# Kernel optimization log

Hardware: AMD Instinct MI355X
Metric: run time of the kernel (lower is better)

The kernel has to match this reference:

```python
import jax, jax.numpy as jnp
import numpy as np

B, L, C = 2, 4096, 1024
H, WIN = 16, 128            # num_heads, window_size (each side)
D = C // H                  # head_dim = 64


def setup_inputs() -> dict:
    key = jax.random.key(0)
    ks = jax.random.split(key, 9)
    s = 0.02
    return {
        "x": jax.random.normal(ks[0], (B, L, C), jnp.float32),
        # Linear weights stored as [in, out] (y = x @ W + b), same math as torch Linear.
        "wq": jax.random.normal(ks[1], (C, C), jnp.float32) * s,
        "bq": jnp.zeros((C,), jnp.float32),
        "wk": jax.random.normal(ks[2], (C, C), jnp.float32) * s,
        "bk": jnp.zeros((C,), jnp.float32),
        "wv": jax.random.normal(ks[3], (C, C), jnp.float32) * s,
        "bv": jnp.zeros((C,), jnp.float32),
        "wo": jax.random.normal(ks[4], (C, C), jnp.float32) * s,
        "bo": jnp.zeros((C,), jnp.float32),
    }


def reference(x, wq, bq, wk, bk, wv, bv, wo, bo):
    b, l, c = x.shape
    nb = l // WIN

    def heads(t):  # (B,L,C) -> (B,H,L,D)
        return t.reshape(b, l, H, D).transpose(0, 2, 1, 3)

    q = heads(x @ wq + bq)
    k = heads(x @ wk + bk)
    v = heads(x @ wv + bv)

    # and ARE included in the softmax, exactly as the original module does).
    kp = jnp.pad(k, ((0, 0), (0, 0), (WIN, WIN), (0, 0)))
    vp = jnp.pad(v, ((0, 0), (0, 0), (WIN, WIN), (0, 0)))

    idx = np.arange(nb)[:, None] * WIN + np.arange(3 * WIN)[None, :]  # [nb, 3W]
    kb = kp[:, :, idx]  # [B,H,nb,3W,D]
    vb = vp[:, :, idx]  # [B,H,nb,3W,D]
    qb = q.reshape(b, H, nb, WIN, D)

    scores = jnp.einsum('bhnqd,bhnkd->bhnqk', qb, kb) / float(np.sqrt(D))
    r = np.arange(WIN)[:, None]
    col = np.arange(3 * WIN)[None, :]
    band = jnp.asarray(np.abs(col - r - WIN) <= WIN)
    scores = jnp.where(band, scores, -jnp.inf)
    probs = jax.nn.softmax(scores, axis=-1)

    out = jnp.einsum('bhnqk,bhnkd->bhnqd', probs, vb)
    out = out.reshape(b, H, l, D).transpose(0, 2, 1, 3).reshape(b, l, c)
    return out @ wo + bo
```

## Files before the change

### kernel.cpp

```cpp
#include <hip/hip_runtime.h>

using short8  = __attribute__((ext_vector_type(8))) short;
using short4v = __attribute__((ext_vector_type(4))) short;
using floatx4 = __attribute__((ext_vector_type(4))) float;

#define MFMA_B16(a, b, c) __builtin_amdgcn_mfma_f32_16x16x32_bf16(a, b, c, 0, 0, 0)

__device__ __forceinline__ short f2bf(float f) {
  union { float f; unsigned u; } v; v.f = f;
  unsigned r = v.u + 0x7fffu + ((v.u >> 16) & 1u);
  return (short)(r >> 16);
}

__device__ __forceinline__ void gload_lds16(const short* g, short* l) {
  __builtin_amdgcn_global_load_lds(
      (const __attribute__((address_space(1))) unsigned int*)g,
      (__attribute__((address_space(3))) unsigned int*)l, 16, 0, 0);
}

__global__ __launch_bounds__(256) void cast_x(const float4* __restrict__ x,
                                              short4v* __restrict__ xb, int n4) {
  int i = blockIdx.x * 256 + threadIdx.x;
  if (i < n4) {
    float4 v = x[i];
    short4v o = { f2bf(v.x), f2bf(v.y), f2bf(v.z), f2bf(v.w) };
    xb[i] = o;
  }
}

__global__ __launch_bounds__(256) void transpose_cast_w(
    const float* __restrict__ w0, const float* __restrict__ w1,
    const float* __restrict__ w2, const float* __restrict__ w3,
    short* __restrict__ wT) {
  __shared__ float tile[32][33];
  int z = blockIdx.z;
  const float* w = z == 0 ? w0 : (z == 1 ? w1 : (z == 2 ? w2 : w3));
  short* out = wT + (size_t)z * 1024 * 1024;
  int n0 = blockIdx.x * 32, k0 = blockIdx.y * 32;
  int tx = threadIdx.x, ty = threadIdx.y;
#pragma unroll
  for (int i = 0; i < 4; ++i)
    tile[ty + i * 8][tx] = w[(size_t)(k0 + ty + i * 8) * 1024 + n0 + tx];
  __syncthreads();
#pragma unroll
  for (int i = 0; i < 4; ++i)
    out[(size_t)(n0 + ty + i * 8) * 1024 + k0 + tx] = f2bf(tile[tx][ty + i * 8]);
}

__global__ __launch_bounds__(256) void gemm_qkv(
    const short* __restrict__ xb, const short* __restrict__ wT,
    const float* __restrict__ bq, const float* __restrict__ bk,
    const float* __restrict__ bv, short* __restrict__ qkv) {
  const int K = 1024;
  int z = blockIdx.z;
  const short* wt = wT + (size_t)z * 1024 * 1024;
  const float* bias = z == 0 ? bq : (z == 1 ? bk : bv);
  short* out = qkv + (size_t)z * 8192 * 1024;

  int m0 = blockIdx.x * 128, n0 = blockIdx.y * 128;
  __shared__ __align__(16) short a[128][32];
  __shared__ __align__(16) short bt[128][32];
  int tid = threadIdx.x;
  int w = tid >> 6, lane = tid & 63, quad = lane >> 4, l16 = lane & 15;
  int wm = (w >> 1) * 64, wn = (w & 1) * 64;
  floatx4 zf = {0.f, 0.f, 0.f, 0.f};
  floatx4 acc[4][4];
#pragma unroll
  for (int i = 0; i < 4; ++i)
#pragma unroll
    for (int j = 0; j < 4; ++j) acc[i][j] = zf;

  int rowL = lane >> 2;
  int segL = (lane & 3) * 8;
  const short* ga = xb + (size_t)(m0 + w * 32 + rowL) * K + segL;
  const short* gb = wt + (size_t)(n0 + w * 32 + rowL) * K + segL;
  short* la = &a[w * 32][0];
  short* lb = &bt[w * 32][0];

  for (int k0 = 0; k0 < K; k0 += 32) {
    __syncthreads();
    gload_lds16(ga + k0, la);
    gload_lds16(ga + (size_t)16 * K + k0, la + 16 * 32);
    gload_lds16(gb + k0, lb);
    gload_lds16(gb + (size_t)16 * K + k0, lb + 16 * 32);
    __syncthreads();
    short8 af[4], bf[4];
#pragma unroll
    for (int t = 0; t < 4; ++t) {
      af[t] = *(const short8*)(&a[wm + t * 16 + l16][quad * 8]);
      bf[t] = *(const short8*)(&bt[wn + t * 16 + l16][quad * 8]);
    }
#pragma unroll
    for (int i = 0; i < 4; ++i)
#pragma unroll
      for (int j = 0; j < 4; ++j)
        acc[i][j] = MFMA_B16(af[i], bf[j], acc[i][j]);
  }

  if (z == 2) {
#pragma unroll
    for (int i = 0; i < 4; ++i)
#pragma unroll
      for (int j = 0; j < 4; ++j) {
        int m = m0 + wm + i * 16 + quad * 4;
        int cc = n0 + wn + j * 16 + l16;
        float bs = bias[cc];
        int b = m >> 12, l = m & 4095;
        int hh = cc >> 6, d = cc & 63;
        short4v pack;
#pragma unroll
        for (int rg = 0; rg < 4; ++rg) pack[rg] = f2bf(acc[i][j][rg] + bs);
        *(short4v*)(out + ((size_t)(b * 16 + hh) * 64 + d) * 4096 + l) = pack;
      }
  } else {
    float qs = (z == 0) ? 0.125f : 1.0f;
#pragma unroll
    for (int i = 0; i < 4; ++i)
#pragma unroll
      for (int j = 0; j < 4; ++j)
#pragma unroll
        for (int rg = 0; rg < 4; ++rg) {
          int m = m0 + wm + i * 16 + quad * 4 + rg;
          int cc = n0 + wn + j * 16 + l16;
          float v = (acc[i][j][rg] + bias[cc]) * qs;
          int b = m >> 12, l = m & 4095;
          int hh = cc >> 6, d = cc & 63;
          out[((size_t)(b * 16 + hh) * 4096 + l) * 64 + d] = f2bf(v);
        }
  }
}

__global__ __launch_bounds__(256) void attn_kern(const short* __restrict__ qkv,
                                                 short* __restrict__ attnb) {
  const int L = 4096, H = 16;
  int n = blockIdx.x, h = blockIdx.y, b = blockIdx.z;
  const size_t hs = (size_t)L * 64;
  const short* Qp = qkv + (size_t)(b * H + h) * hs;
  const short* Kp = qkv + (size_t)8192 * 1024 + (size_t)(b * H + h) * hs;
  const short* Vt = qkv + (size_t)2 * 8192 * 1024 + (size_t)(b * H + h) * hs;

  __shared__ __align__(16) short kt[128][72];
  __shared__ __align__(16) short vt[80][136];
  __shared__ __align__(16) short pl[4][32][136];

  int tid = threadIdx.x, w = tid >> 6, lane = tid & 63, quad = lane >> 4, l16 = lane & 15;

  for (int i = tid; i < 16 * 136; i += 256) {
    int rr = i / 136;
    vt[64 + rr][i - rr * 136] = (rr == 0) ? (short)0x3F80 : (short)0;
  }

  short8 qf[2][2];
#pragma unroll
  for (int rt = 0; rt < 2; ++rt)
#pragma unroll
    for (int ks = 0; ks < 2; ++ks)
      qf[rt][ks] = *(const short8*)(Qp + (size_t)(n * 128 + w * 32 + rt * 16 + l16) * 64 + ks * 32 + quad * 8);

  floatx4 zf = {0.f, 0.f, 0.f, 0.f};
  floatx4 o[2][4];
  floatx4 osum[2];
#pragma unroll
  for (int i = 0; i < 2; ++i) {
    osum[i] = zf;
#pragma unroll
    for (int j = 0; j < 4; ++j) o[i][j] = zf;
  }

#pragma unroll
  for (int c = 0; c < 3; ++c) {
    int bk = n - 1 + c;
    bool inr = (c == 1) || (c == 0 ? (n > 0) : (n < 31));
    __syncthreads();
    if (inr) {
      const short* kc_ = Kp + (size_t)bk * 128 * 64;
      int kr = tid >> 2, ksg = (tid & 3) * 16;
#pragma unroll
      for (int p = 0; p < 2; ++p) {
        int r2 = p * 64 + kr;
        *(short8*)(&kt[r2][ksg])     = *(const short8*)(kc_ + r2 * 64 + ksg);
        *(short8*)(&kt[r2][ksg + 8]) = *(const short8*)(kc_ + r2 * 64 + ksg + 8);
      }
      const short* vc_ = Vt + (size_t)bk * 128;
      int vr = tid >> 2, vsg = (tid & 3) * 32;
#pragma unroll
      for (int q2 = 0; q2 < 4; ++q2)
        *(short8*)(&vt[vr][vsg + q2 * 8]) = *(const short8*)(vc_ + (size_t)vr * 4096 + vsg + q2 * 8);
    } else {
      short8 z8 = {0, 0, 0, 0, 0, 0, 0, 0};
      int kr = tid >> 2, ksg = (tid & 3) * 16;
#pragma unroll
      for (int p = 0; p < 2; ++p) {
        int r2 = p * 64 + kr;
        *(short8*)(&kt[r2][ksg])     = z8;
        *(short8*)(&kt[r2][ksg + 8]) = z8;
      }
      int vr = tid >> 2, vsg = (tid & 3) * 32;
#pragma unroll
      for (int q2 = 0; q2 < 4; ++q2) *(short8*)(&vt[vr][vsg + q2 * 8]) = z8;
    }
    __syncthreads();

    floatx4 s[2][8];
#pragma unroll
    for (int rt = 0; rt < 2; ++rt)
#pragma unroll
      for (int ct = 0; ct < 8; ++ct) s[rt][ct] = zf;
#pragma unroll
    for (int ct = 0; ct < 8; ++ct) {
      short8 kf0 = *(const short8*)(&kt[ct * 16 + l16][quad * 8]);
      short8 kf1 = *(const short8*)(&kt[ct * 16 + l16][32 + quad * 8]);
#pragma unroll
      for (int rt = 0; rt < 2; ++rt) {
        s[rt][ct] = MFMA_B16(qf[rt][0], kf0, s[rt][ct]);
        s[rt][ct] = MFMA_B16(qf[rt][1], kf1, s[rt][ct]);
      }
    }

#pragma unroll
    for (int rt = 0; rt < 2; ++rt) {
#pragma unroll
      for (int rg = 0; rg < 4; ++rg) {
        int r = w * 32 + rt * 16 + quad * 4 + rg;
#pragma unroll
        for (int ct = 0; ct < 8; ++ct) {
          int j = ct * 16 + l16;
          float p = __expf(s[rt][ct][rg]);
          if (c == 0) p = (j < r) ? 0.f : p;
          if (c == 2) p = (j > r) ? 0.f : p;
          pl[w][rt * 16 + quad * 4 + rg][ct * 16 + l16] = f2bf(p);
        }
      }
    }

#pragma unroll
    for (int ks = 0; ks < 4; ++ks) {
      short8 vf[5];
#pragma unroll
      for (int ct = 0; ct < 4; ++ct)
        vf[ct] = *(const short8*)(&vt[ct * 16 + l16][ks * 32 + quad * 8]);
      vf[4] = *(const short8*)(&vt[64 + l16][ks * 32 + quad * 8]);
#pragma unroll
      for (int rt = 0; rt < 2; ++rt) {
        short8 pf = *(const short8*)(&pl[w][rt * 16 + l16][ks * 32 + quad * 8]);
#pragma unroll
        for (int ct = 0; ct < 4; ++ct) o[rt][ct] = MFMA_B16(pf, vf[ct], o[rt][ct]);
        osum[rt] = MFMA_B16(pf, vf[4], osum[rt]);
      }
    }
  }

#pragma unroll
  for (int rt = 0; rt < 2; ++rt) {
#pragma unroll
    for (int rg = 0; rg < 4; ++rg) {
      float ssum = __shfl(osum[rt][rg], lane & 48);
      float inv = 1.f / ssum;
      int r = n * 128 + w * 32 + rt * 16 + quad * 4 + rg;
#pragma unroll
      for (int ct = 0; ct < 4; ++ct)
        attnb[(size_t)(b * L + r) * 1024 + h * 64 + ct * 16 + l16] =
            f2bf(o[rt][ct][rg] * inv);
    }
  }
}

__global__ __launch_bounds__(256) void gemm_out(
    const short* __restrict__ attnb, const short* __restrict__ wTo,
    const float* __restrict__ bo, float* __restrict__ outp) {
  const int K = 1024;
  int m0 = blockIdx.x * 128, n0 = blockIdx.y * 128;
  __shared__ __align__(16) short a[128][32];
  __shared__ __align__(16) short bt[128][32];
  int tid = threadIdx.x;
  int w = tid >> 6, lane = tid & 63, quad = lane >> 4, l16 = lane & 15;
  int wm = (w >> 1) * 64, wn = (w & 1) * 64;
  floatx4 zf = {0.f, 0.f, 0.f, 0.f};
  floatx4 acc[4][4];
#pragma unroll
  for (int i = 0; i < 4; ++i)
#pragma unroll
    for (int j = 0; j < 4; ++j) acc[i][j] = zf;

  int rowL = lane >> 2;
  int segL = (lane & 3) * 8;
  const short* ga = attnb + (size_t)(m0 + w * 32 + rowL) * K + segL;
  const short* gb = wTo + (size_t)(n0 + w * 32 + rowL) * K + segL;
  short* la = &a[w * 32][0];
  short* lb = &bt[w * 32][0];

  for (int k0 = 0; k0 < K; k0 += 32) {
    __syncthreads();
    gload_lds16(ga + k0, la);
    gload_lds16(ga + (size_t)16 * K + k0, la + 16 * 32);
    gload_lds16(gb + k0, lb);
    gload_lds16(gb + (size_t)16 * K + k0, lb + 16 * 32);
    __syncthreads();
    short8 af[4], bf[4];
#pragma unroll
    for (int t = 0; t < 4; ++t) {
      af[t] = *(const short8*)(&a[wm + t * 16 + l16][quad * 8]);
      bf[t] = *(const short8*)(&bt[wn + t * 16 + l16][quad * 8]);
    }
#pragma unroll
    for (int i = 0; i < 4; ++i)
#pragma unroll
      for (int j = 0; j < 4; ++j)
        acc[i][j] = MFMA_B16(af[i], bf[j], acc[i][j]);
  }
#pragma unroll
  for (int i = 0; i < 4; ++i)
#pragma unroll
    for (int j = 0; j < 4; ++j)
#pragma unroll
      for (int rg = 0; rg < 4; ++rg) {
        int m = m0 + wm + i * 16 + quad * 4 + rg;
        int c = n0 + wn + j * 16 + l16;
        outp[(size_t)m * 1024 + c] = acc[i][j][rg] + bo[c];
      }
}

extern "C" void kernel_launch(void* const* d_in, const int* in_sizes, int n_in,
                              void* d_out, int out_size, void* d_ws, size_t ws_size,
                              hipStream_t stream) {
  const float* x  = (const float*)d_in[0];
  const float* wq = (const float*)d_in[1];
  const float* bq = (const float*)d_in[2];
  const float* wk = (const float*)d_in[3];
  const float* bk = (const float*)d_in[4];
  const float* wv = (const float*)d_in[5];
  const float* bv = (const float*)d_in[6];
  const float* wo = (const float*)d_in[7];
  const float* bo = (const float*)d_in[8];

  char* ws = (char*)d_ws;
  short* xb    = (short*)ws;
  short* wT    = (short*)(ws + (16u << 20));
  short* qkv   = (short*)(ws + (24u << 20));
  short* attnb = (short*)(ws + (72u << 20));

  cast_x<<<8192, 256, 0, stream>>>((const float4*)x, (short4v*)xb, 2097152);
  transpose_cast_w<<<dim3(32, 32, 4), dim3(32, 8), 0, stream>>>(wq, wk, wv, wo, wT);
  gemm_qkv<<<dim3(64, 8, 3), 256, 0, stream>>>(xb, wT, bq, bk, bv, qkv);
  attn_kern<<<dim3(32, 16, 2), 256, 0, stream>>>(qkv, attnb);
  gemm_out<<<dim3(64, 8), 256, 0, stream>>>(attnb, wT + 3u * 1024 * 1024, bo, (float*)d_out);
}
```

Baseline: 236.4 us.

## Merge prep kernels, transpose V separately, skip masked attention tiles

Fuses the x cast and the weight transpose-cast into one launch. V is now written row-major by the QKV GEMM and then transposed by a separate LDS-tiled kernel, replacing the scattered short4 stores. The attention kernel skips QK and PV MFMAs and exp work for tiles that are fully masked in the edge chunks, and writes a register-resident ones fragment for the row-sum instead of keeping it in LDS. It adds an extra launch and an extra V round trip through memory, plus a __syncthreads in the attention loop.

```diff
diff --git a/kernel.cpp b/kernel.cpp
--- a/kernel.cpp
+++ b/kernel.cpp
@@ -18,44 +18,45 @@
       (__attribute__((address_space(3))) unsigned int*)l, 16, 0, 0);
 }
 
-__global__ __launch_bounds__(256) void cast_x(const float4* __restrict__ x,
-                                              short4v* __restrict__ xb, int n4) {
-  int i = blockIdx.x * 256 + threadIdx.x;
-  if (i < n4) {
-    float4 v = x[i];
-    short4v o = { f2bf(v.x), f2bf(v.y), f2bf(v.z), f2bf(v.w) };
-    xb[i] = o;
-  }
-}
-
-__global__ __launch_bounds__(256) void transpose_cast_w(
+__global__ __launch_bounds__(256) void prep(
+    const float4* __restrict__ x, short4v* __restrict__ xb,
     const float* __restrict__ w0, const float* __restrict__ w1,
     const float* __restrict__ w2, const float* __restrict__ w3,
     short* __restrict__ wT) {
   __shared__ float tile[32][33];
-  int z = blockIdx.z;
-  const float* w = z == 0 ? w0 : (z == 1 ? w1 : (z == 2 ? w2 : w3));
-  short* out = wT + (size_t)z * 1024 * 1024;
-  int n0 = blockIdx.x * 32, k0 = blockIdx.y * 32;
-  int tx = threadIdx.x, ty = threadIdx.y;
-#pragma unroll
-  for (int i = 0; i < 4; ++i)
-    tile[ty + i * 8][tx] = w[(size_t)(k0 + ty + i * 8) * 1024 + n0 + tx];
-  __syncthreads();
-#pragma unroll
-  for (int i = 0; i < 4; ++i)
-    out[(size_t)(n0 + ty + i * 8) * 1024 + k0 + tx] = f2bf(tile[tx][ty + i * 8]);
+  int blk = blockIdx.x;
+  if (blk < 8192) {
+    int i = blk * 256 + threadIdx.x;
+    float4 v = x[i];
+    short4v o = { f2bf(v.x), f2bf(v.y), f2bf(v.z), f2bf(v.w) };
+    xb[i] = o;
+  } else {
+    int r = blk - 8192;
+    int z = r >> 10; r &= 1023;
+    const float* w = z == 0 ? w0 : (z == 1 ? w1 : (z == 2 ? w2 : w3));
+    short* out = wT + (size_t)z * 1024 * 1024;
+    int n0 = (r & 31) * 32, k0 = (r >> 5) * 32;
+    int tx = threadIdx.x & 31, ty = threadIdx.x >> 5;
+#pragma unroll
+    for (int i = 0; i < 4; ++i)
+      tile[ty + i * 8][tx] = w[(size_t)(k0 + ty + i * 8) * 1024 + n0 + tx];
+    __syncthreads();
+#pragma unroll
+    for (int i = 0; i < 4; ++i)
+      out[(size_t)(n0 + ty + i * 8) * 1024 + k0 + tx] = f2bf(tile[tx][ty + i * 8]);
+  }
 }
 
 __global__ __launch_bounds__(256) void gemm_qkv(
     const short* __restrict__ xb, const short* __restrict__ wT,
     const float* __restrict__ bq, const float* __restrict__ bk,
-    const float* __restrict__ bv, short* __restrict__ qkv) {
+    const float* __restrict__ bv, short* __restrict__ qkv,
+    short* __restrict__ vstage) {
   const int K = 1024;
   int z = blockIdx.z;
   const short* wt = wT + (size_t)z * 1024 * 1024;
   const float* bias = z == 0 ? bq : (z == 1 ? bk : bv);
-  short* out = qkv + (size_t)z * 8192 * 1024;
+  short* out = (z == 2) ? vstage : qkv + (size_t)z * 8192 * 1024;
 
   int m0 = blockIdx.x * 128, n0 = blockIdx.y * 128;
   __shared__ __align__(16) short a[128][32];
@@ -97,37 +98,39 @@
         acc[i][j] = MFMA_B16(af[i], bf[j], acc[i][j]);
   }
 
-  if (z == 2) {
-#pragma unroll
-    for (int i = 0; i < 4; ++i)
-#pragma unroll
-      for (int j = 0; j < 4; ++j) {
-        int m = m0 + wm + i * 16 + quad * 4;
+  float qs = (z == 0) ? 0.125f : 1.0f;
+#pragma unroll
+  for (int i = 0; i < 4; ++i)
+#pragma unroll
+    for (int j = 0; j < 4; ++j)
+#pragma unroll
+      for (int rg = 0; rg < 4; ++rg) {
+        int m = m0 + wm + i * 16 + quad * 4 + rg;
         int cc = n0 + wn + j * 16 + l16;
-        float bs = bias[cc];
+        float v = (acc[i][j][rg] + bias[cc]) * qs;
         int b = m >> 12, l = m & 4095;
         int hh = cc >> 6, d = cc & 63;
-        short4v pack;
-#pragma unroll
-        for (int rg = 0; rg < 4; ++rg) pack[rg] = f2bf(acc[i][j][rg] + bs);
-        *(short4v*)(out + ((size_t)(b * 16 + hh) * 64 + d) * 4096 + l) = pack;
-      }
-  } else {
-    float qs = (z == 0) ? 0.125f : 1.0f;
-#pragma unroll
-    for (int i = 0; i < 4; ++i)
-#pragma unroll
-      for (int j = 0; j < 4; ++j)
-#pragma unroll
-        for (int rg = 0; rg < 4; ++rg) {
-          int m = m0 + wm + i * 16 + quad * 4 + rg;
-          int cc = n0 + wn + j * 16 + l16;
-          float v = (acc[i][j][rg] + bias[cc]) * qs;
-          int b = m >> 12, l = m & 4095;
-          int hh = cc >> 6, d = cc & 63;
-          out[((size_t)(b * 16 + hh) * 4096 + l) * 64 + d] = f2bf(v);
-        }
-  }
+        out[((size_t)(b * 16 + hh) * 4096 + l) * 64 + d] = f2bf(v);
+      }
+}
+
+__global__ __launch_bounds__(256) void transpose_v(const short* __restrict__ vin,
+                                                   short* __restrict__ vout) {
+  __shared__ __align__(16) short t[64][72];
+  int bh = blockIdx.x >> 6;
+  int l0 = (blockIdx.x & 63) * 64;
+  const short* src = vin + ((size_t)bh * 4096 + l0) * 64;
+  int tid = threadIdx.x;
+  int row = tid >> 2, seg = (tid & 3) * 16;
+  *(short8*)(&t[row][seg])     = *(const short8*)(src + row * 64 + seg);
+  *(short8*)(&t[row][seg + 8]) = *(const short8*)(src + row * 64 + seg + 8);
+  __syncthreads();
+  short* dst = vout + (size_t)bh * 64 * 4096 + l0;
+  short8 p0, p1;
+#pragma unroll
+  for (int j = 0; j < 8; ++j) { p0[j] = t[seg + j][row]; p1[j] = t[seg + 8 + j][row]; }
+  *(short8*)(dst + (size_t)row * 4096 + seg)     = p0;
+  *(short8*)(dst + (size_t)row * 4096 + seg + 8) = p1;
 }
 
 __global__ __launch_bounds__(256) void attn_kern(const short* __restrict__ qkv,
@@ -140,14 +143,16 @@
   const short* Vt = qkv + (size_t)2 * 8192 * 1024 + (size_t)(b * H + h) * hs;
 
   __shared__ __align__(16) short kt[128][72];
-  __shared__ __align__(16) short vt[80][136];
+  __shared__ __align__(16) short vt[64][136];
   __shared__ __align__(16) short pl[4][32][136];
 
   int tid = threadIdx.x, w = tid >> 6, lane = tid & 63, quad = lane >> 4, l16 = lane & 15;
 
-  for (int i = tid; i < 16 * 136; i += 256) {
-    int rr = i / 136;
-    vt[64 + rr][i - rr * 136] = (rr == 0) ? (short)0x3F80 : (short)0;
+  short8 onesf;
+  {
+    short ov = (l16 == 0) ? (short)0x3F80 : (short)0;
+#pragma unroll
+    for (int j = 0; j < 8; ++j) onesf[j] = ov;
   }
 
   short8 qf[2][2];
@@ -208,44 +213,67 @@
       for (int ct = 0; ct < 8; ++ct) s[rt][ct] = zf;
 #pragma unroll
     for (int ct = 0; ct < 8; ++ct) {
-      short8 kf0 = *(const short8*)(&kt[ct * 16 + l16][quad * 8]);
-      short8 kf1 = *(const short8*)(&kt[ct * 16 + l16][32 + quad * 8]);
-#pragma unroll
-      for (int rt = 0; rt < 2; ++rt) {
-        s[rt][ct] = MFMA_B16(qf[rt][0], kf0, s[rt][ct]);
-        s[rt][ct] = MFMA_B16(qf[rt][1], kf1, s[rt][ct]);
+      bool any = (c == 0) ? (ct >= w * 2) : (c == 2) ? (ct <= w * 2 + 1) : true;
+      if (any) {
+        short8 kf0 = *(const short8*)(&kt[ct * 16 + l16][quad * 8]);
+        short8 kf1 = *(const short8*)(&kt[ct * 16 + l16][32 + quad * 8]);
+#pragma unroll
+        for (int rt = 0; rt < 2; ++rt) {
+          bool valid = (c == 0) ? (ct >= w * 2 + rt) : (c == 2) ? (ct <= w * 2 + rt) : true;
+          if (valid) {
+            s[rt][ct] = MFMA_B16(qf[rt][0], kf0, s[rt][ct]);
+            s[rt][ct] = MFMA_B16(qf[rt][1], kf1, s[rt][ct]);
+          }
+        }
       }
     }
 
 #pragma unroll
     for (int rt = 0; rt < 2; ++rt) {
-#pragma unroll
-      for (int rg = 0; rg < 4; ++rg) {
-        int r = w * 32 + rt * 16 + quad * 4 + rg;
-#pragma unroll
-        for (int ct = 0; ct < 8; ++ct) {
-          int j = ct * 16 + l16;
-          float p = __expf(s[rt][ct][rg]);
-          if (c == 0) p = (j < r) ? 0.f : p;
-          if (c == 2) p = (j > r) ? 0.f : p;
-          pl[w][rt * 16 + quad * 4 + rg][ct * 16 + l16] = f2bf(p);
+      int wrt = w * 2 + rt;
+#pragma unroll
+      for (int ct = 0; ct < 8; ++ct) {
+        bool tileMasked = (c == 0) ? (ct < wrt) : (c == 2) ? (ct > wrt) : false;
+        bool ksDead = (c == 0) ? (2 * (ct >> 1) + 1 < wrt)
+                    : (c == 2) ? (2 * (ct >> 1) > wrt) : false;
+        if (ksDead) continue;
+        if (tileMasked) {
+#pragma unroll
+          for (int rg = 0; rg < 4; ++rg)
+            pl[w][rt * 16 + quad * 4 + rg][ct * 16 + l16] = 0;
+        } else {
+#pragma unroll
+          for (int rg = 0; rg < 4; ++rg) {
+            int r = w * 32 + rt * 16 + quad * 4 + rg;
+            int j = ct * 16 + l16;
+            float p = __expf(s[rt][ct][rg]);
+            if (c == 0) p = (j < r) ? 0.f : p;
+            if (c == 2) p = (j > r) ? 0.f : p;
+            pl[w][rt * 16 + quad * 4 + rg][ct * 16 + l16] = f2bf(p);
+          }
         }
       }
     }
 
+    __syncthreads();
+
 #pragma unroll
     for (int ks = 0; ks < 4; ++ks) {
-      short8 vf[5];
+      bool anyrt = (c == 0) ? (2 * ks + 1 >= w * 2) : (c == 2) ? (2 * ks <= w * 2 + 1) : true;
+      if (!anyrt) continue;
+      short8 vf[4];
 #pragma unroll
       for (int ct = 0; ct < 4; ++ct)
         vf[ct] = *(const short8*)(&vt[ct * 16 + l16][ks * 32 + quad * 8]);
-      vf[4] = *(const short8*)(&vt[64 + l16][ks * 32 + quad * 8]);
 #pragma unroll
       for (int rt = 0; rt < 2; ++rt) {
+        int wrt = w * 2 + rt;
+        bool ksDead = (c == 0) ? (2 * ks + 1 < wrt) : (c == 2) ? (2 * ks > wrt) : false;
+        if (ksDead) continue;
         short8 pf = *(const short8*)(&pl[w][rt * 16 + l16][ks * 32 + quad * 8]);
 #pragma unroll
         for (int ct = 0; ct < 4; ++ct) o[rt][ct] = MFMA_B16(pf, vf[ct], o[rt][ct]);
-        osum[rt] = MFMA_B16(pf, vf[4], osum[rt]);
+        osum[rt] = MFMA_B16(pf, onesf, osum[rt]);
       }
     }
   }
@@ -334,14 +362,15 @@
   const float* bo = (const float*)d_in[8];
 
   char* ws = (char*)d_ws;
-  short* xb    = (short*)ws;
-  short* wT    = (short*)(ws + (16u << 20));
-  short* qkv   = (short*)(ws + (24u << 20));
-  short* attnb = (short*)(ws + (72u << 20));
-
-  cast_x<<<8192, 256, 0, stream>>>((const float4*)x, (short4v*)xb, 2097152);
-  transpose_cast_w<<<dim3(32, 32, 4), dim3(32, 8), 0, stream>>>(wq, wk, wv, wo, wT);
-  gemm_qkv<<<dim3(64, 8, 3), 256, 0, stream>>>(xb, wT, bq, bk, bv, qkv);
+  short* xb     = (short*)ws;
+  short* wT     = (short*)(ws + (16u << 20));
+  short* qkv    = (short*)(ws + (24u << 20));
+  short* attnb  = (short*)(ws + (72u << 20));
+  short* vstage = attnb;
+
+  prep<<<12288, 256, 0, stream>>>((const float4*)x, (short4v*)xb, wq, wk, wv, wo, wT);
+  gemm_qkv<<<dim3(64, 8, 3), 256, 0, stream>>>(xb, wT, bq, bk, bv, qkv, vstage);
+  transpose_v<<<2048, 256, 0, stream>>>(vstage, qkv + (size_t)2 * 8192 * 1024);
   attn_kern<<<dim3(32, 16, 2), 256, 0, stream>>>(qkv, attnb);
   gemm_out<<<dim3(64, 8), 256, 0, stream>>>(attnb, wT + 3u * 1024 * 1024, bo, (float*)d_out);
 }
```

Measured after the change: 229.0 us. -3.1%, faster.
